# Kernel optimization log

Hardware: AMD Instinct MI355X
Metric: run time of the kernel (lower is better)

The kernel has to match this reference:

```python
import jax, jax.numpy as jnp
import numpy as np

B, L, D, H = 2, 2048, 1024, 16
HD = D // H


def setup_inputs() -> dict:
    key = jax.random.key(0)
    ks = jax.random.split(key, 12)
    s = 1.0 / np.sqrt(D)
    inp = {
        "q": jax.random.normal(ks[0], (B, L, D), jnp.float32),
        "k": jax.random.normal(ks[1], (B, L, D), jnp.float32),
        "v": jax.random.normal(ks[2], (B, L, D), jnp.float32),
        "mask": jnp.zeros((B, L), dtype=bool),  # True = masked out
        "Wq": jax.random.normal(ks[3], (D, D), jnp.float32) * s,
        "bq": jnp.zeros((D,), jnp.float32),
        "Wk": jax.random.normal(ks[4], (D, D), jnp.float32) * s,
        "bk": jnp.zeros((D,), jnp.float32),
        "Wv": jax.random.normal(ks[5], (D, D), jnp.float32) * s,
        "bv": jnp.zeros((D,), jnp.float32),
        "Wo": jax.random.normal(ks[6], (D, D), jnp.float32) * s,
        "bo": jnp.zeros((D,), jnp.float32),
    }
    return inp


def reference(q, k, v, mask, Wq, bq, Wk, bk, Wv, bv, Wo, bo):
    # linear projections (torch Linear: x @ W.T + b), split into heads: [B,H,L,HD]
    def proj(x, W, b):
        y = jnp.einsum('bld,ed->ble', x, W) + b
        return y.reshape(x.shape[0], x.shape[1], H, HD).transpose(0, 2, 1, 3)

    Q = proj(q, Wq, bq)
    K = proj(k, Wk, bk)
    V = proj(v, Wv, bv)

    scale = 1.0 / np.sqrt(HD).astype(np.float32)
    scores = jnp.einsum('bhqd,bhkd->bhqk', Q, K) * scale  # [B,H,Lq,Lk]
    # mask [B,Lk] -> broadcast over heads and query positions
    scores = jnp.where(mask[:, None, None, :], -jnp.inf, scores)
    attn = jax.nn.softmax(scores, axis=-1)
    out = jnp.einsum('bhqk,bhkd->bhqd', attn, V)  # [B,H,Lq,HD]
    out = out.transpose(0, 2, 1, 3).reshape(q.shape[0], q.shape[1], D)
    return jnp.einsum('bld,ed->ble', out, Wo) + bo
```

## Files before the change

kernel.cpp:

```cpp
#include <hip/hip_runtime.h>

#define LSEQ 2048
#define DMODEL 1024
#define NHEAD 16
#define HDIM 64

typedef __attribute__((ext_vector_type(8))) short bf16x8;
typedef __attribute__((ext_vector_type(4))) float f32x4;
typedef __attribute__((ext_vector_type(16))) float f32x16;
typedef unsigned int u32;
typedef unsigned short u16;

static __device__ __forceinline__ u16 f2bf(float x) {
    return (u16)((__builtin_bit_cast(u32, x) + 0x8000u) >> 16);
}

static __device__ __forceinline__ u32 f2bf_pk(float hi, float lo) {
    u32 a = __builtin_bit_cast(u32, hi) + 0x8000u;
    u32 b = __builtin_bit_cast(u32, lo) + 0x8000u;
#if __has_builtin(__builtin_amdgcn_perm)
    return __builtin_amdgcn_perm(a, b, 0x07060302u);
#else
    return (a & 0xFFFF0000u) | (b >> 16);
#endif
}

static __device__ __forceinline__ float fast_exp2(float x) {
#if __has_builtin(__builtin_amdgcn_exp2f)
    return __builtin_amdgcn_exp2f(x);
#else
    return __expf(x * 0.6931471805599453f);
#endif
}

static __device__ __forceinline__ void gll16(const void* g, void* l) {
    __builtin_amdgcn_global_load_lds(
        (const __attribute__((address_space(1))) u32*)g,
        (__attribute__((address_space(3))) u32*)l, 16, 0, 0);
}

__global__ __launch_bounds__(256) void conv_all(
    const float* __restrict__ q, const float* __restrict__ k, const float* __restrict__ v,
    const float* __restrict__ w0, const float* __restrict__ w1,
    const float* __restrict__ w2, const float* __restrict__ w3,
    u16* __restrict__ Qf, u16* __restrict__ Kf, u16* __restrict__ Vf,
    u16* __restrict__ o0, u16* __restrict__ o1, u16* __restrict__ o2,
    u16* __restrict__ o3) {
    const int bid = blockIdx.x;
    const float* s; u16* d; int off;
    if (bid < 12288) {
        const int z = bid >> 12;
        off = bid & 4095;
        if (z == 0)      { s = q; d = Qf; }
        else if (z == 1) { s = k; d = Kf; }
        else             { s = v; d = Vf; }
    } else {
        const int t = bid - 12288;
        const int z = t >> 10;
        off = t & 1023;
        if (z == 0)      { s = w0; d = o0; }
        else if (z == 1) { s = w1; d = o1; }
        else if (z == 2) { s = w2; d = o2; }
        else             { s = w3; d = o3; }
    }
    const int i = (off * 256 + threadIdx.x) * 4;
    float4 x = *(const float4*)(s + i);
    uint2 r;
    r.x = f2bf_pk(x.y, x.x);
    r.y = f2bf_pk(x.w, x.z);
    *(uint2*)(d + i) = r;
}

template <int OUT_MODE>
__device__ __forceinline__ void mfma_gemm(u16* __restrict__ sm,
                                          const u16* __restrict__ Xb,
                                          const u16* __restrict__ Wb,
                                          const float* __restrict__ bias,
                                          void* __restrict__ Yv, float scale) {
    u16* As = sm;
    u16* Bs = sm + 8192;

    const int tid = threadIdx.x;
    const int wave = tid >> 6, lane = tid & 63;
    const int l16 = lane & 15, quad = lane >> 4;
    const int wm = (wave >> 1) * 64, wn = (wave & 1) * 64;
    const int m0 = blockIdx.x * 128, n0 = blockIdx.y * 128;

    const u16* Xr = Xb + (size_t)(m0 + (tid >> 2)) * DMODEL + (tid & 3) * 8;
    const u16* Wr = Wb + (size_t)(n0 + (tid >> 2)) * DMODEL + (tid & 3) * 8;
    const int t8 = tid * 8;

    auto stage = [&](int k0, int buf) {
        u16* Ab = As + buf * 4096;
        u16* Bb = Bs + buf * 4096;
        gll16(Xr + k0, Ab + t8);
        gll16(Xr + (size_t)64 * DMODEL + k0, Ab + 2048 + t8);
        gll16(Wr + k0, Bb + t8);
        gll16(Wr + (size_t)64 * DMODEL + k0, Bb + 2048 + t8);
    };

    f32x4 acc[4][4];
    #pragma unroll
    for (int i = 0; i < 4; ++i)
        #pragma unroll
        for (int j = 0; j < 4; ++j)
            #pragma unroll
            for (int r = 0; r < 4; ++r) acc[i][j][r] = 0.0f;

    stage(0, 0);
    __syncthreads();

    #pragma unroll 1
    for (int kt = 0; kt < DMODEL / 32; ++kt) {
        const int cur = kt & 1;
        if (kt + 1 < DMODEL / 32) stage((kt + 1) * 32, cur ^ 1);

        const u16* Ac = As + cur * 4096;
        const u16* Bc = Bs + cur * 4096;
        bf16x8 af[4], bf[4];
        #pragma unroll
        for (int mb = 0; mb < 4; ++mb)
            af[mb] = *(const bf16x8*)(Ac + (wm + mb * 16 + l16) * 32 + quad * 8);
        #pragma unroll
        for (int nb = 0; nb < 4; ++nb)
            bf[nb] = *(const bf16x8*)(Bc + (wn + nb * 16 + l16) * 32 + quad * 8);
        #pragma unroll
        for (int mb = 0; mb < 4; ++mb)
            #pragma unroll
            for (int nb = 0; nb < 4; ++nb)
                acc[mb][nb] = __builtin_amdgcn_mfma_f32_16x16x32_bf16(
                    af[mb], bf[nb], acc[mb][nb], 0, 0, 0);

        __syncthreads();
    }

    #pragma unroll
    for (int nb = 0; nb < 4; ++nb) {
        const int n = n0 + wn + nb * 16 + l16;
        const float bn = bias[n];
        #pragma unroll
        for (int mb = 0; mb < 4; ++mb) {
            const int mb0 = m0 + wm + mb * 16 + quad * 4;
            if (OUT_MODE == 2) {
                u16* Y = (u16*)Yv;
                uint2 rr;
                rr.x = f2bf_pk((acc[mb][nb][1] + bn) * scale, (acc[mb][nb][0] + bn) * scale);
                rr.y = f2bf_pk((acc[mb][nb][3] + bn) * scale, (acc[mb][nb][2] + bn) * scale);
                const int bb = mb0 >> 11, l = mb0 & 2047;
                const int h = n >> 6, hd = n & 63;
                *(uint2*)(Y + ((size_t)((bb * NHEAD + h) * HDIM) + hd) * LSEQ + l) = rr;
            } else {
                #pragma unroll
                for (int r = 0; r < 4; ++r) {
                    const int m = mb0 + r;
                    const float val = (acc[mb][nb][r] + bn) * scale;
                    if (OUT_MODE == 0) {
                        u16* Y = (u16*)Yv;
                        const int bb = m >> 11, l = m & 2047;
                        const int h = n >> 6, hd = n & 63;
                        Y[(((size_t)(bb * NHEAD + h) * LSEQ + l) * HDIM) + hd] = f2bf(val);
                    } else {
                        float* Y = (float*)Yv;
                        Y[(size_t)m * DMODEL + n] = val;
                    }
                }
            }
        }
    }
}

#define QSCALE (0.125f * 1.4426950408889634f)

__global__ __launch_bounds__(256) void qkv_gemm(
    const u16* __restrict__ Qf, const u16* __restrict__ Kf, const u16* __restrict__ Vf,
    const u16* __restrict__ Wqb, const u16* __restrict__ Wkb, const u16* __restrict__ Wvb,
    const float* __restrict__ bq, const float* __restrict__ bk, const float* __restrict__ bv,
    u16* __restrict__ Qp, u16* __restrict__ Kp, u16* __restrict__ Vtp) {
    __shared__ alignas(16) u16 sm[16384];
    if (blockIdx.z == 0)      mfma_gemm<0>(sm, Qf, Wqb, bq, (void*)Qp, QSCALE);
    else if (blockIdx.z == 1) mfma_gemm<0>(sm, Kf, Wkb, bk, (void*)Kp, 1.0f);
    else                      mfma_gemm<2>(sm, Vf, Wvb, bv, (void*)Vtp, 1.0f);
}

__global__ __launch_bounds__(256) void out_gemm(
    const u16* __restrict__ AOb, const u16* __restrict__ Wob,
    const float* __restrict__ bo, float* __restrict__ out) {
    __shared__ alignas(16) u16 sm[16384];
    mfma_gemm<1>(sm, AOb, Wob, bo, (void*)out, 1.0f);
}

#define KT 128

__global__ __launch_bounds__(256, 2) void attn_mfma(
    const u16* __restrict__ Qp, const u16* __restrict__ Kp,
    const u16* __restrict__ Vtp, const unsigned char* __restrict__ mask,
    u16* __restrict__ AOb) {
    __shared__ alignas(16) u16 smem[32768];

    const int tid = threadIdx.x;
    const int wave = tid >> 6;
    const int lane = tid & 63;
    const int l32 = lane & 31;
    const int half = lane >> 5;
    const int bh = blockIdx.x;
    const int b = bh >> 4;
    const int h = bh & 15;
    const int q0 = blockIdx.y * 128;
    const int qw = q0 + wave * 32;

    const u16* Qg = Qp + ((size_t)bh * LSEQ + qw) * HDIM;
    const u16* Kg = Kp + (size_t)bh * LSEQ * HDIM;
    const u16* Vtg = Vtp + (size_t)bh * HDIM * LSEQ;
    const unsigned char* mg = mask + (size_t)b * LSEQ;

    bf16x8 qf[4];
    #pragma unroll
    for (int dc = 0; dc < 4; ++dc)
        qf[dc] = *(const bf16x8*)(Qg + (size_t)l32 * HDIM + dc * 16 + half * 8);

    f32x16 o0 = {}, o1 = {};
    const f32x16 zc = {};
    float ls[4] = {0.0f, 0.0f, 0.0f, 0.0f};

    auto stage = [&](int ktile, int buf) {
        const int k0 = ktile * KT;
        u16* Kb = smem + buf * 8192;
        u16* Vb = smem + 16384 + buf * 8192;
        #pragma unroll
        for (int j = 0; j < 4; ++j) {
            const int cid = j * 256 + tid;
            const int key = cid >> 3, pc = cid & 7, c = pc ^ (key & 7);
            gll16(Kg + (size_t)(k0 + key) * HDIM + c * 8, Kb + cid * 8);
        }
        #pragma unroll
        for (int j = 0; j < 4; ++j) {
            const int cid = j * 256 + tid;
            const int d = cid >> 4, pc = cid & 15, c = pc ^ (d & 15);
            gll16(Vtg + (size_t)d * LSEQ + k0 + c * 8, Vb + cid * 8);
        }
    };

    stage(0, 0);

    for (int kt = 0; kt < LSEQ / KT; ++kt) {
        const int cur = kt & 1;
        const u16* Kb = smem + cur * 8192;
        const u16* Vb = smem + 16384 + cur * 8192;
        const int k0 = kt * KT;
        const int mb0 = mg[k0 + lane];
        const int mb1 = mg[k0 + 64 + lane];

        __syncthreads();
        if (kt + 1 < LSEQ / KT) stage(kt + 1, cur ^ 1);

        f32x16 st[4];
        #pragma unroll
        for (int kb = 0; kb < 4; ++kb) {
            const int key = kb * 32 + l32;
            const int phys = half ^ (key & 7);
            bf16x8 kf = *(const bf16x8*)(Kb + key * 64 + phys * 8);
            st[kb] = __builtin_amdgcn_mfma_f32_32x32x16_bf16(kf, qf[0], zc, 0, 0, 0);
        }
        #pragma unroll
        for (int dc = 1; dc < 4; ++dc)
            #pragma unroll
            for (int kb = 0; kb < 4; ++kb) {
                const int key = kb * 32 + l32;
                const int phys = (dc * 2 + half) ^ (key & 7);
                bf16x8 kf = *(const bf16x8*)(Kb + key * 64 + phys * 8);
                st[kb] = __builtin_amdgcn_mfma_f32_32x32x16_bf16(kf, qf[dc], st[kb], 0, 0, 0);
            }

        const unsigned long long anym = __ballot(mb0 | mb1);
        if (anym) {
            const float b0f = mb0 ? -1e30f : 0.0f;
            const float b1f = mb1 ? -1e30f : 0.0f;
            #pragma unroll
            for (int kb = 0; kb < 4; ++kb)
                #pragma unroll
                for (int r = 0; r < 16; ++r) {
                    const int key = kb * 32 + (r & 3) + 8 * (r >> 2) + 4 * half;
                    const float bv = __shfl((kb < 2) ? b0f : b1f, key & 63, 64);
                    st[kb][r] += bv;
                }
        }

        u32 pk[4][8];
        #pragma unroll
        for (int kb = 0; kb < 4; ++kb)
            #pragma unroll
            for (int w = 0; w < 8; ++w) {
                const float plo = fast_exp2(st[kb][2 * w]);
                const float phi = fast_exp2(st[kb][2 * w + 1]);
                ls[kb] += plo + phi;
                pk[kb][w] = f2bf_pk(phi, plo);
            }

        #pragma unroll
        for (int c = 0; c < 8; ++c) {
            const int kb = c >> 1, wb = 4 * (c & 1);
            u32 w4[4];
#if __has_builtin(__builtin_amdgcn_permlane32_swap)
            auto r02 = __builtin_amdgcn_permlane32_swap(
                (int)pk[kb][wb],     (int)pk[kb][wb + 2], false, false);
            auto r13 = __builtin_amdgcn_permlane32_swap(
                (int)pk[kb][wb + 1], (int)pk[kb][wb + 3], false, false);
            w4[0] = (u32)r02[0]; w4[2] = (u32)r02[1];
            w4[1] = (u32)r13[0]; w4[3] = (u32)r13[1];
#else
            const u32 ta = half ? pk[kb][wb] : pk[kb][wb + 2];
            const u32 tb = half ? pk[kb][wb + 1] : pk[kb][wb + 3];
            const u32 xa = __shfl_xor((int)ta, 32, 64);
            const u32 xb = __shfl_xor((int)tb, 32, 64);
            w4[0] = half ? xa : pk[kb][wb];
            w4[1] = half ? xb : pk[kb][wb + 1];
            w4[2] = half ? pk[kb][wb + 2] : xa;
            w4[3] = half ? pk[kb][wb + 3] : xb;
#endif
            bf16x8 pb = __builtin_bit_cast(bf16x8, *(uint4*)w4);
            {
                const int d = l32;
                const int phys = (c * 2 + half) ^ (d & 15);
                bf16x8 va = *(const bf16x8*)(Vb + d * 128 + phys * 8);
                o0 = __builtin_amdgcn_mfma_f32_32x32x16_bf16(va, pb, o0, 0, 0, 0);
            }
            {
                const int d = 32 + l32;
                const int phys = (c * 2 + half) ^ (d & 15);
                bf16x8 va = *(const bf16x8*)(Vb + d * 128 + phys * 8);
                o1 = __builtin_amdgcn_mfma_f32_32x32x16_bf16(va, pb, o1, 0, 0, 0);
            }
        }
    }

    const float l_l = (ls[0] + ls[1]) + (ls[2] + ls[3]);
    const float l_tot = l_l + __shfl_xor(l_l, 32, 64);
    const float inv = 1.0f / l_tot;
    __syncthreads();
    u16* T = smem;
    #pragma unroll
    for (int nb = 0; nb < 2; ++nb)
        #pragma unroll
        for (int rp = 0; rp < 8; ++rp) {
            const int r = rp * 2;
            const int d = nb * 32 + (r & 3) + 8 * (r >> 2) + 4 * half;
            const float vlo = (nb ? o1[r] : o0[r]) * inv;
            const float vhi = (nb ? o1[r + 1] : o0[r + 1]) * inv;
            *(u32*)(T + (wave * 32 + l32) * 72 + d) = f2bf_pk(vhi, vlo);
        }
    __syncthreads();
    #pragma unroll
    for (int i = 0; i < 4; ++i) {
        const int cid = i * 256 + tid;
        const int row = cid >> 3, ch = cid & 7;
        bf16x8 val = *(const bf16x8*)(T + row * 72 + ch * 8);
        *(bf16x8*)(AOb + ((size_t)(b * LSEQ + q0 + row) * DMODEL) + h * HDIM + ch * 8) = val;
    }
}

extern "C" void kernel_launch(void* const* d_in, const int* in_sizes, int n_in,
                              void* d_out, int out_size, void* d_ws, size_t ws_size,
                              hipStream_t stream) {
    (void)in_sizes; (void)n_in; (void)out_size; (void)ws_size;
    const float* q  = (const float*)d_in[0];
    const float* k  = (const float*)d_in[1];
    const float* v  = (const float*)d_in[2];
    const unsigned char* mask = (const unsigned char*)d_in[3];
    const float* Wq = (const float*)d_in[4];
    const float* bq = (const float*)d_in[5];
    const float* Wk = (const float*)d_in[6];
    const float* bk = (const float*)d_in[7];
    const float* Wv = (const float*)d_in[8];
    const float* bv = (const float*)d_in[9];
    const float* Wo = (const float*)d_in[10];
    const float* bo = (const float*)d_in[11];
    float* out = (float*)d_out;

    u16* ws16 = (u16*)d_ws;
    const size_t M4 = (size_t)4 * 1024 * 1024;
    const size_t M1 = (size_t)1024 * 1024;
    u16* Qf  = ws16;
    u16* Kf  = ws16 + M4;
    u16* Vf  = ws16 + 2 * M4;
    u16* Qp  = ws16 + 3 * M4;
    u16* Kp  = ws16 + 4 * M4;
    u16* Vtp = ws16 + 5 * M4;
    u16* AOb = ws16 + 6 * M4;
    u16* Wqb = ws16 + 7 * M4;
    u16* Wkb = ws16 + 7 * M4 + M1;
    u16* Wvb = ws16 + 7 * M4 + 2 * M1;
    u16* Wob = ws16 + 7 * M4 + 3 * M1;

    conv_all<<<dim3(16384), 256, 0, stream>>>(q, k, v, Wq, Wk, Wv, Wo,
                                              Qf, Kf, Vf, Wqb, Wkb, Wvb, Wob);
    qkv_gemm<<<dim3(32, 8, 3), 256, 0, stream>>>(Qf, Kf, Vf, Wqb, Wkb, Wvb,
                                                 bq, bk, bv, Qp, Kp, Vtp);
    attn_mfma<<<dim3(32, 16), 256, 0, stream>>>(Qp, Kp, Vtp, mask, AOb);
    out_gemm<<<dim3(32, 8), 256, 0, stream>>>(AOb, Wob, bo, out);
}
```

Before: 228.1 us.

## Software-pipeline attention loop: overlap PV of previous tile with QK of next

Restructures the attention key loop so the P·V MFMAs for tile kt-1 are issued after the QK^T MFMAs for tile kt, letting the exp/softmax work overlap with matrix ops. V gets a triple-buffered LDS slot (LDS grows from 64KB to 80KB) while K stays double-buffered. The barrier moves to the end of the iteration. The per-tile mask ballot is replaced by a single up-front check of the whole mask row, so the mask path is skipped entirely when nothing is masked. The larger LDS footprint may reduce occupancy below the two blocks per CU requested by the launch bounds, and the carried pk registers add register pressure.

```diff
diff --git a/kernel.cpp b/kernel.cpp
--- a/kernel.cpp
+++ b/kernel.cpp
@@ -10,6 +10,7 @@
 typedef __attribute__((ext_vector_type(16))) float f32x16;
 typedef unsigned int u32;
 typedef unsigned short u16;
+typedef unsigned long long u64;
 
 static __device__ __forceinline__ u16 f2bf(float x) {
     return (u16)((__builtin_bit_cast(u32, x) + 0x8000u) >> 16);
@@ -190,12 +191,13 @@
 }
 
 #define KT 128
+#define NTILE (LSEQ / KT)
 
 __global__ __launch_bounds__(256, 2) void attn_mfma(
     const u16* __restrict__ Qp, const u16* __restrict__ Kp,
     const u16* __restrict__ Vtp, const unsigned char* __restrict__ mask,
     u16* __restrict__ AOb) {
-    __shared__ alignas(16) u16 smem[32768];
+    __shared__ alignas(16) u16 smem[40960];
 
     const int tid = threadIdx.x;
     const int wave = tid >> 6;
@@ -222,16 +224,19 @@
     const f32x16 zc = {};
     float ls[4] = {0.0f, 0.0f, 0.0f, 0.0f};
 
-    auto stage = [&](int ktile, int buf) {
+    auto stageK = [&](int ktile, int slot) {
         const int k0 = ktile * KT;
-        u16* Kb = smem + buf * 8192;
-        u16* Vb = smem + 16384 + buf * 8192;
+        u16* Kb = smem + slot * 8192;
         #pragma unroll
         for (int j = 0; j < 4; ++j) {
             const int cid = j * 256 + tid;
             const int key = cid >> 3, pc = cid & 7, c = pc ^ (key & 7);
             gll16(Kg + (size_t)(k0 + key) * HDIM + c * 8, Kb + cid * 8);
         }
+    };
+    auto stageV = [&](int ktile, int slot) {
+        const int k0 = ktile * KT;
+        u16* Vb = smem + 16384 + slot * 8192;
         #pragma unroll
         for (int j = 0; j < 4; ++j) {
             const int cid = j * 256 + tid;
@@ -240,18 +245,22 @@
         }
     };
 
-    stage(0, 0);
-
-    for (int kt = 0; kt < LSEQ / KT; ++kt) {
-        const int cur = kt & 1;
-        const u16* Kb = smem + cur * 8192;
-        const u16* Vb = smem + 16384 + cur * 8192;
-        const int k0 = kt * KT;
-        const int mb0 = mg[k0 + lane];
-        const int mb1 = mg[k0 + 64 + lane];
-
-        __syncthreads();
-        if (kt + 1 < LSEQ / KT) stage(kt + 1, cur ^ 1);
+    stageK(0, 0); stageV(0, 0);
+
+    const u64* mg8 = (const u64*)mg;
+    const u64 mm = mg8[lane] | mg8[lane + 64] | mg8[lane + 128] | mg8[lane + 192];
+    const bool mask_any = __any((int)(mm != 0ULL));
+
+    __syncthreads();
+
+    u32 pk[4][8];
+
+    for (int kt = 0; kt < NTILE; ++kt) {
+        if (kt + 1 < NTILE) {
+            stageK(kt + 1, (kt + 1) & 1);
+            stageV(kt + 1, (kt + 1) % 3);
+        }
+        const u16* Kb = smem + (kt & 1) * 8192;
 
         f32x16 st[4];
         #pragma unroll
@@ -271,8 +280,32 @@
                 st[kb] = __builtin_amdgcn_mfma_f32_32x32x16_bf16(kf, qf[dc], st[kb], 0, 0, 0);
             }
 
-        const unsigned long long anym = __ballot(mb0 | mb1);
-        if (anym) {
+        if (kt > 0) {
+            const u16* Vbp = smem + 16384 + ((kt + 2) % 3) * 8192;
+            #pragma unroll
+            for (int c = 0; c < 8; ++c) {
+                const int kb = c >> 1, wb = 4 * (c & 1);
+                {
+                    const int d = l32;
+                    const int phys = (c * 2 + half) ^ (d & 15);
+                    bf16x8 va = *(const bf16x8*)(Vbp + d * 128 + phys * 8);
+                    bf16x8 pb = __builtin_bit_cast(bf16x8, *(uint4*)&pk[kb][wb]);
+                    o0 = __builtin_amdgcn_mfma_f32_32x32x16_bf16(va, pb, o0, 0, 0, 0);
+                }
+                {
+                    const int d = 32 + l32;
+                    const int phys = (c * 2 + half) ^ (d & 15);
+                    bf16x8 va = *(const bf16x8*)(Vbp + d * 128 + phys * 8);
+                    bf16x8 pb = __builtin_bit_cast(bf16x8, *(uint4*)&pk[kb][wb]);
+                    o1 = __builtin_amdgcn_mfma_f32_32x32x16_bf16(va, pb, o1, 0, 0, 0);
+                }
+            }
+        }
+
+        if (mask_any) {
+            const int k0 = kt * KT;
+            const int mb0 = mg[k0 + lane];
+            const int mb1 = mg[k0 + 64 + lane];
             const float b0f = mb0 ? -1e30f : 0.0f;
             const float b1f = mb1 ? -1e30f : 0.0f;
             #pragma unroll
@@ -285,7 +318,7 @@
                 }
         }
 
-        u32 pk[4][8];
+        u32 pkn[4][8];
         #pragma unroll
         for (int kb = 0; kb < 4; ++kb)
             #pragma unroll
@@ -293,41 +326,51 @@
                 const float plo = fast_exp2(st[kb][2 * w]);
                 const float phi = fast_exp2(st[kb][2 * w + 1]);
                 ls[kb] += plo + phi;
-                pk[kb][w] = f2bf_pk(phi, plo);
-            }
-
+                pkn[kb][w] = f2bf_pk(phi, plo);
+            }
+        #pragma unroll
+        for (int kb = 0; kb < 4; ++kb)
+            #pragma unroll
+            for (int wb = 0; wb < 8; wb += 4) {
+#if __has_builtin(__builtin_amdgcn_permlane32_swap)
+                auto r02 = __builtin_amdgcn_permlane32_swap(
+                    (int)pkn[kb][wb],     (int)pkn[kb][wb + 2], false, false);
+                auto r13 = __builtin_amdgcn_permlane32_swap(
+                    (int)pkn[kb][wb + 1], (int)pkn[kb][wb + 3], false, false);
+                pk[kb][wb]     = (u32)r02[0]; pk[kb][wb + 2] = (u32)r02[1];
+                pk[kb][wb + 1] = (u32)r13[0]; pk[kb][wb + 3] = (u32)r13[1];
+#else
+                const u32 ta = half ? pkn[kb][wb] : pkn[kb][wb + 2];
+                const u32 tb = half ? pkn[kb][wb + 1] : pkn[kb][wb + 3];
+                const u32 xa = __shfl_xor((int)ta, 32, 64);
+                const u32 xb = __shfl_xor((int)tb, 32, 64);
+                pk[kb][wb]     = half ? xa : pkn[kb][wb];
+                pk[kb][wb + 1] = half ? xb : pkn[kb][wb + 1];
+                pk[kb][wb + 2] = half ? pkn[kb][wb + 2] : xa;
+                pk[kb][wb + 3] = half ? pkn[kb][wb + 3] : xb;
+#endif
+            }
+
+        __syncthreads();
+    }
+
+    {
+        const u16* Vbp = smem + 16384 + ((NTILE - 1) % 3) * 8192;
         #pragma unroll
         for (int c = 0; c < 8; ++c) {
             const int kb = c >> 1, wb = 4 * (c & 1);
-            u32 w4[4];
-#if __has_builtin(__builtin_amdgcn_permlane32_swap)
-            auto r02 = __builtin_amdgcn_permlane32_swap(
-                (int)pk[kb][wb],     (int)pk[kb][wb + 2], false, false);
-            auto r13 = __builtin_amdgcn_permlane32_swap(
-                (int)pk[kb][wb + 1], (int)pk[kb][wb + 3], false, false);
-            w4[0] = (u32)r02[0]; w4[2] = (u32)r02[1];
-            w4[1] = (u32)r13[0]; w4[3] = (u32)r13[1];
-#else
-            const u32 ta = half ? pk[kb][wb] : pk[kb][wb + 2];
-            const u32 tb = half ? pk[kb][wb + 1] : pk[kb][wb + 3];
-            const u32 xa = __shfl_xor((int)ta, 32, 64);
-            const u32 xb = __shfl_xor((int)tb, 32, 64);
-            w4[0] = half ? xa : pk[kb][wb];
-            w4[1] = half ? xb : pk[kb][wb + 1];
-            w4[2] = half ? pk[kb][wb + 2] : xa;
-            w4[3] = half ? pk[kb][wb + 3] : xb;
-#endif
-            bf16x8 pb = __builtin_bit_cast(bf16x8, *(uint4*)w4);
             {
                 const int d = l32;
                 const int phys = (c * 2 + half) ^ (d & 15);
-                bf16x8 va = *(const bf16x8*)(Vb + d * 128 + phys * 8);
+                bf16x8 va = *(const bf16x8*)(Vbp + d * 128 + phys * 8);
+                bf16x8 pb = __builtin_bit_cast(bf16x8, *(uint4*)&pk[kb][wb]);
                 o0 = __builtin_amdgcn_mfma_f32_32x32x16_bf16(va, pb, o0, 0, 0, 0);
             }
             {
                 const int d = 32 + l32;
                 const int phys = (c * 2 + half) ^ (d & 15);
-                bf16x8 va = *(const bf16x8*)(Vb + d * 128 + phys * 8);
+                bf16x8 va = *(const bf16x8*)(Vbp + d * 128 + phys * 8);
+                bf16x8 pb = __builtin_bit_cast(bf16x8, *(uint4*)&pk[kb][wb]);
                 o1 = __builtin_amdgcn_mfma_f32_32x32x16_bf16(va, pb, o1, 0, 0, 0);
             }
         }
```

Result: no change. 228.9 us (+0.4%).
